# Optimization experiments

Hardware: AMD Instinct MI355X
Metric: run time of the kernel (lower is better)

Reference implementation:

```python
import jax, jax.numpy as jnp
import numpy as np

EPS = 1e-6
GROUPS = 32  # min(C//4, 32) with C=256

def group_norm(x, scale, bias):
    B, H, W, C = x.shape
    g = GROUPS
    xg = x.reshape(B, H, W, g, C // g)
    mean = jnp.mean(xg, axis=(1, 2, 4), keepdims=True)
    var = jnp.var(xg, axis=(1, 2, 4), keepdims=True)
    xg = (xg - mean) * jax.lax.rsqrt(var + EPS)
    return xg.reshape(B, H, W, C) * scale + bias

def nin(x, w, b):
    return jnp.einsum('bhwc,cd->bhwd', x, w) + b

def setup_inputs() -> dict:
    key = jax.random.key(0)
    ks = jax.random.split(key, 11)
    B, H, W, C = 8, 64, 64, 256
    s = 1.0 / np.sqrt(C)
    return {
        'x': jax.random.normal(ks[0], (B, H, W, C), jnp.float32),
        'gn_scale': jnp.ones((C,), jnp.float32),
        'gn_bias': jnp.zeros((C,), jnp.float32),
        'Wq': jax.random.normal(ks[1], (C, C), jnp.float32) * s,
        'bq': jnp.zeros((C,), jnp.float32),
        'Wk': jax.random.normal(ks[2], (C, C), jnp.float32) * s,
        'bk': jnp.zeros((C,), jnp.float32),
        'Wv': jax.random.normal(ks[3], (C, C), jnp.float32) * s,
        'bv': jnp.zeros((C,), jnp.float32),
        'Wo': jax.random.normal(ks[4], (C, C), jnp.float32) * s * 0.1,
        'bo': jnp.zeros((C,), jnp.float32),
    }

def reference(x, gn_scale, gn_bias, Wq, bq, Wk, bk, Wv, bv, Wo, bo):
    B, H, W, C = x.shape
    h = group_norm(x, gn_scale, gn_bias)
    q = nin(h, Wq, bq)
    k = nin(h, Wk, bk)
    v = nin(h, Wv, bv)
    w = jnp.einsum('bhwc,bHWc->bhwHW', q, k) * (C ** -0.5)
    w = w.reshape(B, H, W, H * W)
    w = jax.nn.softmax(w, axis=-1)
    w = w.reshape(B, H, W, H, W)
    h = jnp.einsum('bhwHW,bHWc->bhwc', w, v)
    h = nin(h, Wo, bo)
    return x + h
```

## Files before the change

kernel.cpp:

```cpp
#include <hip/hip_runtime.h>
#include <stdint.h>

using short8 = __attribute__((ext_vector_type(8))) short;
using f32x4  = __attribute__((ext_vector_type(4))) float;

#define L2E 1.44269504088896f

static __device__ __forceinline__ unsigned short f2bf(float f) {
  union { float f; uint32_t u; } v; v.f = f;
  uint32_t r = v.u + 0x7fffu + ((v.u >> 16) & 1u);
  return (unsigned short)(r >> 16);
}
static __device__ __forceinline__ float bf2f(unsigned short u) {
  union { uint32_t u; float f; } v; v.u = ((uint32_t)u) << 16;
  return v.f;
}

static __device__ __forceinline__ void gload16(const unsigned short* g, unsigned short* l) {
  __builtin_amdgcn_global_load_lds(
      (const __attribute__((address_space(1))) void*)g,
      (__attribute__((address_space(3))) void*)l, 16, 0, 0);
}

static __device__ __forceinline__ float red_add_lg(float x) {
  x += __shfl_xor(x, 16);
  x += __shfl_xor(x, 32);
  return x;
}
static __device__ __forceinline__ float red_max_lg(float x) {
  x = fmaxf(x, __shfl_xor(x, 16));
  x = fmaxf(x, __shfl_xor(x, 32));
  return x;
}

__global__ __launch_bounds__(256) void prep_w(
    const float* __restrict__ Wq, const float* __restrict__ Wk,
    const float* __restrict__ Wv, const float* __restrict__ Wo,
    unsigned short* __restrict__ Wt) {
  int k = threadIdx.x, d = blockIdx.x, w = blockIdx.y;
  const float* src = (w==0)?Wq:(w==1)?Wk:(w==2)?Wv:Wo;
  Wt[w*65536 + d*256 + k] = f2bf(src[k*256 + d]);
}

__global__ __launch_bounds__(256) void gn_stats(
    const float* __restrict__ x, float* __restrict__ part) {
  int c = threadIdx.x, ch = blockIdx.x, b = blockIdx.y;
  float s = 0.f, q = 0.f;
  const float* p = x + ((b*4096) + ch*64)*256 + c;
  for (int it = 0; it < 64; ++it) {
    float v = p[it*256];
    s += v; q += v*v;
  }
  s += __shfl_xor(s,1); q += __shfl_xor(q,1);
  s += __shfl_xor(s,2); q += __shfl_xor(q,2);
  s += __shfl_xor(s,4); q += __shfl_xor(q,4);
  if ((c & 7) == 0) {
    int g = c >> 3;
    part[((b*64 + ch)*32 + g)*2 + 0] = s;
    part[((b*64 + ch)*32 + g)*2 + 1] = q;
  }
}

__global__ __launch_bounds__(256) void gn_apply(
    const float* __restrict__ x, const float* __restrict__ part,
    const float* __restrict__ sc, const float* __restrict__ bi,
    unsigned short* __restrict__ h) {
  int c = threadIdx.x, ch = blockIdx.x, b = blockIdx.y;
  int g = c >> 3;
  float s = 0.f, q = 0.f;
  for (int cc = 0; cc < 64; ++cc) {
    s += part[((b*64 + cc)*32 + g)*2 + 0];
    q += part[((b*64 + cc)*32 + g)*2 + 1];
  }
  float mean = s * (1.f/32768.f);
  float var  = q * (1.f/32768.f) - mean*mean;
  float rstd = rsqrtf(var + 1e-6f);
  float a  = rstd * sc[c];
  float d0 = bi[c] - mean * a;
  const float* p = x + ((b*4096) + ch*64)*256 + c;
  unsigned short* o = h + ((b*4096) + ch*64)*256 + c;
  for (int it = 0; it < 64; ++it)
    o[it*256] = f2bf(p[it*256] * a + d0);
}

__global__ __launch_bounds__(256) void gemm_qk(
    const unsigned short* __restrict__ A,
    const unsigned short* __restrict__ Wtq,
    const unsigned short* __restrict__ Wtk,
    const float* __restrict__ bq,
    const float* __restrict__ bk,
    unsigned short* __restrict__ Qout,
    unsigned short* __restrict__ Kout) {
  int tid = threadIdx.x;
  int w = tid >> 6, l = tid & 63, lr = l & 15, lg = l >> 4;
  int i0 = blockIdx.x * 64;
  int j0 = w * 64;
  f32x4 accq[4][4] = {}, acck[4][4] = {};
#pragma unroll
  for (int kk = 0; kk < 8; ++kk) {
    short8 af[4], bfq[4], bfk[4];
#pragma unroll
    for (int mi = 0; mi < 4; ++mi)
      af[mi] = *(const short8*)(A + (i0 + mi*16 + lr)*256 + kk*32 + lg*8);
#pragma unroll
    for (int ni = 0; ni < 4; ++ni) {
      bfq[ni] = *(const short8*)(Wtq + (j0 + ni*16 + lr)*256 + kk*32 + lg*8);
      bfk[ni] = *(const short8*)(Wtk + (j0 + ni*16 + lr)*256 + kk*32 + lg*8);
    }
#pragma unroll
    for (int mi = 0; mi < 4; ++mi)
#pragma unroll
      for (int ni = 0; ni < 4; ++ni) {
        accq[mi][ni] = __builtin_amdgcn_mfma_f32_16x16x32_bf16(af[mi], bfq[ni], accq[mi][ni], 0,0,0);
        acck[mi][ni] = __builtin_amdgcn_mfma_f32_16x16x32_bf16(af[mi], bfk[ni], acck[mi][ni], 0,0,0);
      }
  }
#pragma unroll
  for (int mi = 0; mi < 4; ++mi) {
#pragma unroll
    for (int ni = 0; ni < 4; ++ni) {
      int j = j0 + ni*16 + lr;
#pragma unroll
      for (int r = 0; r < 4; ++r) {
        int i = i0 + mi*16 + lg*4 + r;
        Qout[i*256 + j] = f2bf((accq[mi][ni][r] + bq[j]) * 0.0625f);
        Kout[i*256 + j] = f2bf(acck[mi][ni][r] + bk[j]);
      }
    }
  }
}

__global__ __launch_bounds__(256) void gemm_bt(
    const unsigned short* __restrict__ A,
    const unsigned short* __restrict__ Bm,
    const float* __restrict__ bias_n,
    const float* __restrict__ bias_m,
    const float* __restrict__ resid,
    void* __restrict__ outp, float scale, int mode) {
  int tid = threadIdx.x;
  int w = tid >> 6, l = tid & 63, lr = l & 15, lg = l >> 4;
  int i0 = blockIdx.x * 64;
  int j0 = blockIdx.y * 256 + w * 64;
  f32x4 acc[4][4] = {};
#pragma unroll
  for (int kk = 0; kk < 8; ++kk) {
    short8 af[4], bfr[4];
#pragma unroll
    for (int mi = 0; mi < 4; ++mi)
      af[mi] = *(const short8*)(A + (i0 + mi*16 + lr)*256 + kk*32 + lg*8);
#pragma unroll
    for (int ni = 0; ni < 4; ++ni)
      bfr[ni] = *(const short8*)(Bm + (j0 + ni*16 + lr)*256 + kk*32 + lg*8);
#pragma unroll
    for (int mi = 0; mi < 4; ++mi)
#pragma unroll
      for (int ni = 0; ni < 4; ++ni)
        acc[mi][ni] = __builtin_amdgcn_mfma_f32_16x16x32_bf16(af[mi], bfr[ni], acc[mi][ni], 0,0,0);
  }
#pragma unroll
  for (int mi = 0; mi < 4; ++mi) {
#pragma unroll
    for (int ni = 0; ni < 4; ++ni) {
      int j = j0 + ni*16 + lr;
#pragma unroll
      for (int r = 0; r < 4; ++r) {
        int i = i0 + mi*16 + lg*4 + r;
        float v = acc[mi][ni][r];
        if (mode == 0) {
          ((unsigned short*)outp)[i*256 + j] = f2bf((v + bias_n[j]) * scale);
        } else if (mode == 1) {
          int idx = ((j >> 12) << 20) + i*4096 + (j & 4095);
          ((unsigned short*)outp)[idx] = f2bf(v + bias_m[i]);
        } else {
          ((float*)outp)[i*256 + j] = v + bias_n[j] + resid[i*256 + j];
        }
      }
    }
  }
}

static __device__ __forceinline__ void stage_kv32(
    const unsigned short* __restrict__ Kb, const unsigned short* __restrict__ Vb,
    int kt, unsigned short* dK, unsigned short* dV, int w, int l) {
#pragma unroll
  for (int i = 0; i < 4; ++i) {
    int t = (w*4 + i)*64 + l;
    int r = t >> 5, cs = t & 31;
    int cg = cs ^ (r & 7);
    gload16(Kb + (kt*32 + r)*256 + cg*8, dK + t*8);
  }
#pragma unroll
  for (int i = 0; i < 4; ++i) {
    int t = (w*4 + i)*64 + l;
    int d = t >> 2, s = t & 3;
    int sg = s ^ ((d ^ (d >> 2)) & 3);
    gload16(Vb + d*4096 + kt*32 + sg*8, dV + t*8);
  }
}

__global__ __launch_bounds__(256, 2) void attn_fwd(
    const unsigned short* __restrict__ Q,
    const unsigned short* __restrict__ Kmat,
    const unsigned short* __restrict__ Vt,
    unsigned short* __restrict__ P0,
    unsigned short* __restrict__ P1,
    float* __restrict__ stats) {
  __shared__ __align__(16) unsigned short ldsK[2][32][256];
  __shared__ __align__(16) unsigned short ldsV[2][256][32];

  int tid = threadIdx.x;
  int w = tid >> 6, l = tid & 63, lr = l & 15, lg = l >> 4;
  int b  = blockIdx.x & 7;
  int mt = (blockIdx.x >> 3) & 31;
  int ks = blockIdx.x >> 8;
  int m0 = mt*128 + w*32;
  int sw = lr & 7;
  int vsw = (lr ^ (lr >> 2)) & 3;
  int lgp = ((lg & 1) << 1) | (lg >> 1);

  const unsigned short* Kb = Kmat + b*(4096*256) + ks*(2048*256);
  const unsigned short* Vb = Vt   + (b << 20) + ks*2048;
  unsigned short* Pp = ks ? P1 : P0;

  short8 qf[2][8];
#pragma unroll
  for (int qn = 0; qn < 2; ++qn) {
    int qbase = ((b*4096) + m0 + qn*16 + lr)*256 + lg*8;
#pragma unroll
    for (int kk = 0; kk < 8; ++kk)
      qf[qn][kk] = *(const short8*)(Q + qbase + kk*32);
  }

  float mrun[2], lrun[2];
  f32x4 oacc[2][16] = {};
  mrun[0] = mrun[1] = -1e30f;
  lrun[0] = lrun[1] = 0.f;

  stage_kv32(Kb, Vb, 0, &ldsK[0][0][0], &ldsV[0][0][0], w, l);

  for (int kt = 0; kt < 64; ++kt) {
    int cur = kt & 1;
    if (kt < 63) {
      stage_kv32(Kb, Vb, kt+1, &ldsK[cur^1][0][0], &ldsV[cur^1][0][0], w, l);
      asm volatile("s_waitcnt vmcnt(8)" ::: "memory");
    } else {
      asm volatile("s_waitcnt vmcnt(0)" ::: "memory");
    }
    __builtin_amdgcn_s_barrier();
    __builtin_amdgcn_sched_barrier(0);

    const unsigned short (*Kc)[256] = ldsK[cur];
    const unsigned short (*Vc)[32]  = ldsV[cur];

    f32x4 s_[2][2];
#pragma unroll
    for (int qn = 0; qn < 2; ++qn)
#pragma unroll
      for (int kn = 0; kn < 2; ++kn) s_[qn][kn] = (f32x4){0.f,0.f,0.f,0.f};
#pragma unroll
    for (int kn = 0; kn < 2; ++kn) {
#pragma unroll
      for (int kk = 0; kk < 8; ++kk) {
        short8 kf = *(const short8*)&Kc[kn*16 + lr][((kk*4 + lg) ^ sw)*8];
        s_[0][kn] = __builtin_amdgcn_mfma_f32_16x16x32_bf16(kf, qf[0][kk], s_[0][kn], 0,0,0);
        s_[1][kn] = __builtin_amdgcn_mfma_f32_16x16x32_bf16(kf, qf[1][kk], s_[1][kn], 0,0,0);
      }
    }

    short8 pa[2];
#pragma unroll
    for (int qn = 0; qn < 2; ++qn) {
      float ma = fmaxf(fmaxf(s_[qn][0][0], s_[qn][0][1]), fmaxf(s_[qn][0][2], s_[qn][0][3]));
      float mb = fmaxf(fmaxf(s_[qn][1][0], s_[qn][1][1]), fmaxf(s_[qn][1][2], s_[qn][1][3]));
      float pmax = fmaxf(ma, mb);
      if (__any(pmax > mrun[qn] + 8.f)) {
        float mx = red_max_lg(pmax);
        float mnew = fmaxf(mrun[qn], mx);
        float alpha = __builtin_amdgcn_exp2f((mrun[qn] - mnew) * L2E);
        mrun[qn] = mnew;
        lrun[qn] *= alpha;
        float at[4];
#pragma unroll
        for (int r = 0; r < 4; ++r) at[r] = __shfl(alpha, lg*4 + r);
#pragma unroll
        for (int jt = 0; jt < 16; ++jt)
#pragma unroll
          for (int r = 0; r < 4; ++r) oacc[qn][jt][r] *= at[r];
      }
      float mL = mrun[qn] * L2E;
      float p[2][4];
#pragma unroll
      for (int kn = 0; kn < 2; ++kn)
#pragma unroll
        for (int r = 0; r < 4; ++r)
          p[kn][r] = __builtin_amdgcn_exp2f(s_[qn][kn][r]*L2E - mL);
      float t0 = (p[0][0]+p[0][1]) + (p[0][2]+p[0][3]);
      float t1 = (p[1][0]+p[1][1]) + (p[1][2]+p[1][3]);
      lrun[qn] += red_add_lg(t0 + t1);
      unsigned int X0, X1, Y0, Y1;
      asm("v_cvt_pk_bf16_f32 %0, %1, %2" : "=v"(X0) : "v"(p[0][0]), "v"(p[0][1]));
      asm("v_cvt_pk_bf16_f32 %0, %1, %2" : "=v"(X1) : "v"(p[0][2]), "v"(p[0][3]));
      asm("v_cvt_pk_bf16_f32 %0, %1, %2" : "=v"(Y0) : "v"(p[1][0]), "v"(p[1][1]));
      asm("v_cvt_pk_bf16_f32 %0, %1, %2" : "=v"(Y1) : "v"(p[1][2]), "v"(p[1][3]));
      asm("v_permlane16_swap_b32 %0, %1" : "+v"(X0), "+v"(Y0));
      asm("v_permlane16_swap_b32 %0, %1" : "+v"(X1), "+v"(Y1));
      union { unsigned int u[4]; short8 s8; } pk;
      pk.u[0] = X0;
      pk.u[1] = X1;
      pk.u[2] = Y0;
      pk.u[3] = Y1;
      pa[qn] = pk.s8;
    }

#pragma unroll
    for (int jt = 0; jt < 16; ++jt) {
      short8 vf = *(const short8*)&Vc[jt*16 + lr][(lgp ^ vsw)*8];
      oacc[0][jt] = __builtin_amdgcn_mfma_f32_16x16x32_bf16(pa[0], vf, oacc[0][jt], 0,0,0);
      oacc[1][jt] = __builtin_amdgcn_mfma_f32_16x16x32_bf16(pa[1], vf, oacc[1][jt], 0,0,0);
    }
    __builtin_amdgcn_sched_barrier(0);
    __builtin_amdgcn_s_barrier();
  }

  if (lg == 0) {
#pragma unroll
    for (int qn = 0; qn < 2; ++qn) {
      int row = b*4096 + m0 + qn*16 + lr;
      stats[(ks*32768 + row)*2 + 0] = mrun[qn];
      stats[(ks*32768 + row)*2 + 1] = lrun[qn];
    }
  }
#pragma unroll
  for (int qn = 0; qn < 2; ++qn) {
#pragma unroll
    for (int r = 0; r < 4; ++r) {
      int row = ((b*4096) + m0 + qn*16 + lg*4 + r)*256;
#pragma unroll
      for (int jt = 0; jt < 16; ++jt)
        Pp[row + jt*16 + lr] = f2bf(oacc[qn][jt][r]);
    }
  }
}

__global__ __launch_bounds__(256) void merge_attn(
    const unsigned short* __restrict__ P0,
    const unsigned short* __restrict__ P1,
    const float* __restrict__ stats,
    unsigned short* __restrict__ Out) {
  int tid = threadIdx.x;
  int row = blockIdx.x*8 + (tid >> 5);
  int c8  = (tid & 31) * 8;
  float m1 = stats[row*2 + 0],          l1 = stats[row*2 + 1];
  float m2 = stats[(32768 + row)*2 + 0], l2 = stats[(32768 + row)*2 + 1];
  float M  = fmaxf(m1, m2);
  float a1 = __builtin_amdgcn_exp2f((m1 - M) * L2E);
  float a2 = __builtin_amdgcn_exp2f((m2 - M) * L2E);
  float inv = 1.f / (a1*l1 + a2*l2);
  a1 *= inv; a2 *= inv;
  short8 v1 = *(const short8*)(P0 + row*256 + c8);
  short8 v2 = *(const short8*)(P1 + row*256 + c8);
  union { unsigned short u[8]; short8 s8; } o;
#pragma unroll
  for (int j = 0; j < 8; ++j)
    o.u[j] = f2bf(bf2f((unsigned short)v1[j])*a1 + bf2f((unsigned short)v2[j])*a2);
  *(short8*)(Out + row*256 + c8) = o.s8;
}

extern "C" void kernel_launch(void* const* d_in, const int* in_sizes, int n_in,
                              void* d_out, int out_size, void* d_ws, size_t ws_size,
                              hipStream_t stream) {
  (void)in_sizes; (void)n_in; (void)out_size; (void)ws_size;
  const float* x  = (const float*)d_in[0];
  const float* gs = (const float*)d_in[1];
  const float* gb = (const float*)d_in[2];
  const float* Wq = (const float*)d_in[3];
  const float* bq = (const float*)d_in[4];
  const float* Wk = (const float*)d_in[5];
  const float* bk = (const float*)d_in[6];
  const float* Wv = (const float*)d_in[7];
  const float* bv = (const float*)d_in[8];
  const float* Wo = (const float*)d_in[9];
  const float* bo = (const float*)d_in[10];

  char* ws = (char*)d_ws;
  unsigned short* h  = (unsigned short*)(ws);
  unsigned short* Qb = (unsigned short*)(ws + (size_t)16777216);
  unsigned short* Kb = (unsigned short*)(ws + (size_t)33554432);
  unsigned short* Vt = (unsigned short*)(ws + (size_t)50331648);
  unsigned short* Wt = (unsigned short*)(ws + (size_t)67108864);
  float* part        = (float*)(ws + (size_t)67108864 + 524288);
  float* stats       = (float*)(ws + (size_t)67108864 + 524288 + 131072);
  unsigned short* Op1 = (unsigned short*)d_out;

  prep_w  <<<dim3(256,4), 256, 0, stream>>>(Wq, Wk, Wv, Wo, Wt);
  gn_stats<<<dim3(64,8),  256, 0, stream>>>(x, part);
  gn_apply<<<dim3(64,8),  256, 0, stream>>>(x, part, gs, gb, h);
  gemm_qk<<<dim3(512,1), 256, 0, stream>>>(h, Wt, Wt+65536, bq, bk, Qb, Kb);
  gemm_bt<<<dim3(4,128), 256, 0, stream>>>(Wt+131072, h, nullptr, bv, nullptr, Vt, 1.0f, 1);
  attn_fwd<<<dim3(512),  256, 0, stream>>>(Qb, Kb, Vt, h, Op1, stats);
  merge_attn<<<dim3(4096), 256, 0, stream>>>(h, Op1, stats, Qb);
  gemm_bt<<<dim3(512,1), 256, 0, stream>>>(Qb, Wt+196608, bo, nullptr, x, d_out, 1.0f, 2);
}
```

Baseline: 325.6 us.

## Fuse group-norm apply into QK and V projection GEMM operand loads

Replaces the gn_apply kernel, which wrote a normalized bf16 copy of the activations, with a tiny per-batch coefficient kernel. The QK and V projection GEMMs now read fp32 x directly and apply the scale/shift and bf16 conversion while building MFMA fragments. This removes one full write and re-read of the normalized tensor, at the cost of reading fp32 (twice the bytes) in both GEMMs. The attention kernel also precomputes its K/V staging offsets once instead of recomputing them each tile.

```diff
diff --git a/kernel.cpp b/kernel.cpp
--- a/kernel.cpp
+++ b/kernel.cpp
@@ -31,6 +31,28 @@
   x = fmaxf(x, __shfl_xor(x, 16));
   x = fmaxf(x, __shfl_xor(x, 32));
   return x;
+}
+
+static __device__ __forceinline__ short8 gn_frag(
+    const float* __restrict__ xp, f32x4 ca0, f32x4 ca1, f32x4 cd0, f32x4 cd1) {
+  f32x4 x0 = *(const f32x4*)xp;
+  f32x4 x1 = *(const f32x4*)(xp + 4);
+  float g0 = fmaf(x0[0], ca0[0], cd0[0]);
+  float g1 = fmaf(x0[1], ca0[1], cd0[1]);
+  float g2 = fmaf(x0[2], ca0[2], cd0[2]);
+  float g3 = fmaf(x0[3], ca0[3], cd0[3]);
+  float g4 = fmaf(x1[0], ca1[0], cd1[0]);
+  float g5 = fmaf(x1[1], ca1[1], cd1[1]);
+  float g6 = fmaf(x1[2], ca1[2], cd1[2]);
+  float g7 = fmaf(x1[3], ca1[3], cd1[3]);
+  unsigned int u0, u1, u2, u3;
+  asm("v_cvt_pk_bf16_f32 %0, %1, %2" : "=v"(u0) : "v"(g0), "v"(g1));
+  asm("v_cvt_pk_bf16_f32 %0, %1, %2" : "=v"(u1) : "v"(g2), "v"(g3));
+  asm("v_cvt_pk_bf16_f32 %0, %1, %2" : "=v"(u2) : "v"(g4), "v"(g5));
+  asm("v_cvt_pk_bf16_f32 %0, %1, %2" : "=v"(u3) : "v"(g6), "v"(g7));
+  union { unsigned int u[4]; short8 s8; } pk;
+  pk.u[0] = u0; pk.u[1] = u1; pk.u[2] = u2; pk.u[3] = u3;
+  return pk.s8;
 }
 
 __global__ __launch_bounds__(256) void prep_w(
@@ -61,11 +83,11 @@
   }
 }
 
-__global__ __launch_bounds__(256) void gn_apply(
-    const float* __restrict__ x, const float* __restrict__ part,
+__global__ __launch_bounds__(256) void gn_coef(
+    const float* __restrict__ part,
     const float* __restrict__ sc, const float* __restrict__ bi,
-    unsigned short* __restrict__ h) {
-  int c = threadIdx.x, ch = blockIdx.x, b = blockIdx.y;
+    float* __restrict__ agn, float* __restrict__ dgn) {
+  int c = threadIdx.x, b = blockIdx.x;
   int g = c >> 3;
   float s = 0.f, q = 0.f;
   for (int cc = 0; cc < 64; ++cc) {
@@ -76,44 +98,144 @@
   float var  = q * (1.f/32768.f) - mean*mean;
   float rstd = rsqrtf(var + 1e-6f);
   float a  = rstd * sc[c];
-  float d0 = bi[c] - mean * a;
-  const float* p = x + ((b*4096) + ch*64)*256 + c;
-  unsigned short* o = h + ((b*4096) + ch*64)*256 + c;
-  for (int it = 0; it < 64; ++it)
-    o[it*256] = f2bf(p[it*256] * a + d0);
+  agn[b*256 + c] = a;
+  dgn[b*256 + c] = bi[c] - mean * a;
 }
 
 __global__ __launch_bounds__(256) void gemm_qk(
-    const unsigned short* __restrict__ A,
+    const float* __restrict__ x,
+    const float* __restrict__ agn, const float* __restrict__ dgn,
     const unsigned short* __restrict__ Wtq,
     const unsigned short* __restrict__ Wtk,
     const float* __restrict__ bq,
     const float* __restrict__ bk,
     unsigned short* __restrict__ Qout,
     unsigned short* __restrict__ Kout) {
+  __shared__ float aco[256], dco[256];
+  int tid = threadIdx.x;
+  int w = tid >> 6, l = tid & 63, lr = l & 15, lg = l >> 4;
+  int i0 = blockIdx.x * 64;
+  int b  = blockIdx.x >> 6;
+  int j0 = w * 64;
+  aco[tid] = agn[b*256 + tid];
+  dco[tid] = dgn[b*256 + tid];
+  __syncthreads();
+  f32x4 accq[4][4] = {}, acck[4][4] = {};
+#pragma unroll
+  for (int kk = 0; kk < 8; ++kk) {
+    int k0 = kk*32 + lg*8;
+    f32x4 ca0 = *(const f32x4*)&aco[k0];
+    f32x4 ca1 = *(const f32x4*)&aco[k0 + 4];
+    f32x4 cd0 = *(const f32x4*)&dco[k0];
+    f32x4 cd1 = *(const f32x4*)&dco[k0 + 4];
+    short8 af[4], bfq[4], bfk[4];
+#pragma unroll
+    for (int mi = 0; mi < 4; ++mi)
+      af[mi] = gn_frag(x + (i0 + mi*16 + lr)*256 + k0, ca0, ca1, cd0, cd1);
+#pragma unroll
+    for (int ni = 0; ni < 4; ++ni) {
+      bfq[ni] = *(const short8*)(Wtq + (j0 + ni*16 + lr)*256 + k0);
+      bfk[ni] = *(const short8*)(Wtk + (j0 + ni*16 + lr)*256 + k0);
+    }
+#pragma unroll
+    for (int mi = 0; mi < 4; ++mi)
+#pragma unroll
+      for (int ni = 0; ni < 4; ++ni) {
+        accq[mi][ni] = __builtin_amdgcn_mfma_f32_16x16x32_bf16(af[mi], bfq[ni], accq[mi][ni], 0,0,0);
+        acck[mi][ni] = __builtin_amdgcn_mfma_f32_16x16x32_bf16(af[mi], bfk[ni], acck[mi][ni], 0,0,0);
+      }
+  }
+#pragma unroll
+  for (int mi = 0; mi < 4; ++mi) {
+#pragma unroll
+    for (int ni = 0; ni < 4; ++ni) {
+      int j = j0 + ni*16 + lr;
+#pragma unroll
+      for (int r = 0; r < 4; ++r) {
+        int i = i0 + mi*16 + lg*4 + r;
+        Qout[i*256 + j] = f2bf((accq[mi][ni][r] + bq[j]) * 0.0625f);
+        Kout[i*256 + j] = f2bf(acck[mi][ni][r] + bk[j]);
+      }
+    }
+  }
+}
+
+__global__ __launch_bounds__(256) void gemm_vt(
+    const unsigned short* __restrict__ Wtv,
+    const float* __restrict__ x,
+    const float* __restrict__ agn, const float* __restrict__ dgn,
+    const float* __restrict__ bv,
+    unsigned short* __restrict__ Vt) {
+  __shared__ float aco[256], dco[256];
+  int tid = threadIdx.x;
+  int w = tid >> 6, l = tid & 63, lr = l & 15, lg = l >> 4;
+  int i0 = blockIdx.x * 64;
+  int j0 = blockIdx.y * 256 + w * 64;
+  int b  = blockIdx.y >> 4;
+  aco[tid] = agn[b*256 + tid];
+  dco[tid] = dgn[b*256 + tid];
+  __syncthreads();
+  f32x4 acc[4][4] = {};
+#pragma unroll
+  for (int kk = 0; kk < 8; ++kk) {
+    int k0 = kk*32 + lg*8;
+    f32x4 ca0 = *(const f32x4*)&aco[k0];
+    f32x4 ca1 = *(const f32x4*)&aco[k0 + 4];
+    f32x4 cd0 = *(const f32x4*)&dco[k0];
+    f32x4 cd1 = *(const f32x4*)&dco[k0 + 4];
+    short8 af[4], bfr[4];
+#pragma unroll
+    for (int mi = 0; mi < 4; ++mi)
+      af[mi] = *(const short8*)(Wtv + (i0 + mi*16 + lr)*256 + k0);
+#pragma unroll
+    for (int ni = 0; ni < 4; ++ni)
+      bfr[ni] = gn_frag(x + (j0 + ni*16 + lr)*256 + k0, ca0, ca1, cd0, cd1);
+#pragma unroll
+    for (int mi = 0; mi < 4; ++mi)
+#pragma unroll
+      for (int ni = 0; ni < 4; ++ni)
+        acc[mi][ni] = __builtin_amdgcn_mfma_f32_16x16x32_bf16(af[mi], bfr[ni], acc[mi][ni], 0,0,0);
+  }
+#pragma unroll
+  for (int mi = 0; mi < 4; ++mi) {
+#pragma unroll
+    for (int ni = 0; ni < 4; ++ni) {
+      int j = j0 + ni*16 + lr;
+#pragma unroll
+      for (int r = 0; r < 4; ++r) {
+        int i = i0 + mi*16 + lg*4 + r;
+        int idx = ((j >> 12) << 20) + i*4096 + (j & 4095);
+        Vt[idx] = f2bf(acc[mi][ni][r] + bv[i]);
+      }
+    }
+  }
+}
+
+__global__ __launch_bounds__(256) void gemm_bt(
+    const unsigned short* __restrict__ A,
+    const unsigned short* __restrict__ Bm,
+    const float* __restrict__ bias_n,
+    const float* __restrict__ resid,
+    float* __restrict__ outp) {
   int tid = threadIdx.x;
   int w = tid >> 6, l = tid & 63, lr = l & 15, lg = l >> 4;
   int i0 = blockIdx.x * 64;
   int j0 = w * 64;
-  f32x4 accq[4][4] = {}, acck[4][4] = {};
+  f32x4 acc[4][4] = {};
 #pragma unroll
   for (int kk = 0; kk < 8; ++kk) {
-    short8 af[4], bfq[4], bfk[4];
+    short8 af[4], bfr[4];
 #pragma unroll
     for (int mi = 0; mi < 4; ++mi)
       af[mi] = *(const short8*)(A + (i0 + mi*16 + lr)*256 + kk*32 + lg*8);
 #pragma unroll
-    for (int ni = 0; ni < 4; ++ni) {
-      bfq[ni] = *(const short8*)(Wtq + (j0 + ni*16 + lr)*256 + kk*32 + lg*8);
-      bfk[ni] = *(const short8*)(Wtk + (j0 + ni*16 + lr)*256 + kk*32 + lg*8);
-    }
-#pragma unroll
-    for (int mi = 0; mi < 4; ++mi)
-#pragma unroll
-      for (int ni = 0; ni < 4; ++ni) {
-        accq[mi][ni] = __builtin_amdgcn_mfma_f32_16x16x32_bf16(af[mi], bfq[ni], accq[mi][ni], 0,0,0);
-        acck[mi][ni] = __builtin_amdgcn_mfma_f32_16x16x32_bf16(af[mi], bfk[ni], acck[mi][ni], 0,0,0);
-      }
+    for (int ni = 0; ni < 4; ++ni)
+      bfr[ni] = *(const short8*)(Bm + (j0 + ni*16 + lr)*256 + kk*32 + lg*8);
+#pragma unroll
+    for (int mi = 0; mi < 4; ++mi)
+#pragma unroll
+      for (int ni = 0; ni < 4; ++ni)
+        acc[mi][ni] = __builtin_amdgcn_mfma_f32_16x16x32_bf16(af[mi], bfr[ni], acc[mi][ni], 0,0,0);
   }
 #pragma unroll
   for (int mi = 0; mi < 4; ++mi) {
@@ -123,78 +245,9 @@
 #pragma unroll
       for (int r = 0; r < 4; ++r) {
         int i = i0 + mi*16 + lg*4 + r;
-        Qout[i*256 + j] = f2bf((accq[mi][ni][r] + bq[j]) * 0.0625f);
-        Kout[i*256 + j] = f2bf(acck[mi][ni][r] + bk[j]);
-      }
-    }
-  }
-}
-
-__global__ __launch_bounds__(256) void gemm_bt(
-    const unsigned short* __restrict__ A,
-    const unsigned short* __restrict__ Bm,
-    const float* __restrict__ bias_n,
-    const float* __restrict__ bias_m,
-    const float* __restrict__ resid,
-    void* __restrict__ outp, float scale, int mode) {
-  int tid = threadIdx.x;
-  int w = tid >> 6, l = tid & 63, lr = l & 15, lg = l >> 4;
-  int i0 = blockIdx.x * 64;
-  int j0 = blockIdx.y * 256 + w * 64;
-  f32x4 acc[4][4] = {};
-#pragma unroll
-  for (int kk = 0; kk < 8; ++kk) {
-    short8 af[4], bfr[4];
-#pragma unroll
-    for (int mi = 0; mi < 4; ++mi)
-      af[mi] = *(const short8*)(A + (i0 + mi*16 + lr)*256 + kk*32 + lg*8);
-#pragma unroll
-    for (int ni = 0; ni < 4; ++ni)
-      bfr[ni] = *(const short8*)(Bm + (j0 + ni*16 + lr)*256 + kk*32 + lg*8);
-#pragma unroll
-    for (int mi = 0; mi < 4; ++mi)
-#pragma unroll
-      for (int ni = 0; ni < 4; ++ni)
-        acc[mi][ni] = __builtin_amdgcn_mfma_f32_16x16x32_bf16(af[mi], bfr[ni], acc[mi][ni], 0,0,0);
-  }
-#pragma unroll
-  for (int mi = 0; mi < 4; ++mi) {
-#pragma unroll
-    for (int ni = 0; ni < 4; ++ni) {
-      int j = j0 + ni*16 + lr;
-#pragma unroll
-      for (int r = 0; r < 4; ++r) {
-        int i = i0 + mi*16 + lg*4 + r;
-        float v = acc[mi][ni][r];
-        if (mode == 0) {
-          ((unsigned short*)outp)[i*256 + j] = f2bf((v + bias_n[j]) * scale);
-        } else if (mode == 1) {
-          int idx = ((j >> 12) << 20) + i*4096 + (j & 4095);
-          ((unsigned short*)outp)[idx] = f2bf(v + bias_m[i]);
-        } else {
-          ((float*)outp)[i*256 + j] = v + bias_n[j] + resid[i*256 + j];
-        }
-      }
-    }
-  }
-}
-
-static __device__ __forceinline__ void stage_kv32(
-    const unsigned short* __restrict__ Kb, const unsigned short* __restrict__ Vb,
-    int kt, unsigned short* dK, unsigned short* dV, int w, int l) {
-#pragma unroll
-  for (int i = 0; i < 4; ++i) {
-    int t = (w*4 + i)*64 + l;
-    int r = t >> 5, cs = t & 31;
-    int cg = cs ^ (r & 7);
-    gload16(Kb + (kt*32 + r)*256 + cg*8, dK + t*8);
-  }
-#pragma unroll
-  for (int i = 0; i < 4; ++i) {
-    int t = (w*4 + i)*64 + l;
-    int d = t >> 2, s = t & 3;
-    int sg = s ^ ((d ^ (d >> 2)) & 3);
-    gload16(Vb + d*4096 + kt*32 + sg*8, dV + t*8);
+        outp[i*256 + j] = acc[mi][ni][r] + bias_n[j] + resid[i*256 + j];
+      }
+    }
   }
 }
 
@@ -222,6 +275,17 @@
   const unsigned short* Vb = Vt   + (b << 20) + ks*2048;
   unsigned short* Pp = ks ? P1 : P0;
 
+  int koff[4], voff[4], dst[4];
+#pragma unroll
+  for (int i = 0; i < 4; ++i) {
+    int t = (w*4 + i)*64 + l;
+    int r = t >> 5, cs = t & 31;
+    koff[i] = r*256 + (cs ^ (r & 7))*8;
+    int d = t >> 2, s = t & 3;
+    voff[i] = d*4096 + (s ^ ((d ^ (d >> 2)) & 3))*8;
+    dst[i]  = t*8;
+  }
+
   short8 qf[2][8];
 #pragma unroll
   for (int qn = 0; qn < 2; ++qn) {
@@ -236,12 +300,22 @@
   mrun[0] = mrun[1] = -1e30f;
   lrun[0] = lrun[1] = 0.f;
 
-  stage_kv32(Kb, Vb, 0, &ldsK[0][0][0], &ldsV[0][0][0], w, l);
+#pragma unroll
+  for (int i = 0; i < 4; ++i) gload16(Kb + koff[i], &ldsK[0][0][0] + dst[i]);
+#pragma unroll
+  for (int i = 0; i < 4; ++i) gload16(Vb + voff[i], &ldsV[0][0][0] + dst[i]);
 
   for (int kt = 0; kt < 64; ++kt) {
     int cur = kt & 1;
     if (kt < 63) {
-      stage_kv32(Kb, Vb, kt+1, &ldsK[cur^1][0][0], &ldsV[cur^1][0][0], w, l);
+      const unsigned short* Kn = Kb + (kt + 1)*8192;
+      const unsigned short* Vn = Vb + (kt + 1)*32;
+      unsigned short* dK = &ldsK[cur^1][0][0];
+      unsigned short* dV = &ldsV[cur^1][0][0];
+#pragma unroll
+      for (int i = 0; i < 4; ++i) gload16(Kn + koff[i], dK + dst[i]);
+#pragma unroll
+      for (int i = 0; i < 4; ++i) gload16(Vn + voff[i], dV + dst[i]);
       asm volatile("s_waitcnt vmcnt(8)" ::: "memory");
     } else {
       asm volatile("s_waitcnt vmcnt(0)" ::: "memory");
@@ -305,10 +379,7 @@
       asm("v_permlane16_swap_b32 %0, %1" : "+v"(X0), "+v"(Y0));
       asm("v_permlane16_swap_b32 %0, %1" : "+v"(X1), "+v"(Y1));
       union { unsigned int u[4]; short8 s8; } pk;
-      pk.u[0] = X0;
-      pk.u[1] = X1;
-      pk.u[2] = Y0;
-      pk.u[3] = Y1;
+      pk.u[0] = X0; pk.u[1] = X1; pk.u[2] = Y0; pk.u[3] = Y1;
       pa[qn] = pk.s8;
     }
 
@@ -390,14 +461,16 @@
   unsigned short* Wt = (unsigned short*)(ws + (size_t)67108864);
   float* part        = (float*)(ws + (size_t)67108864 + 524288);
   float* stats       = (float*)(ws + (size_t)67108864 + 524288 + 131072);
+  float* agn = (float*)ws;
+  float* dgn = (float*)(ws + 8192);
   unsigned short* Op1 = (unsigned short*)d_out;
 
   prep_w  <<<dim3(256,4), 256, 0, stream>>>(Wq, Wk, Wv, Wo, Wt);
   gn_stats<<<dim3(64,8),  256, 0, stream>>>(x, part);
-  gn_apply<<<dim3(64,8),  256, 0, stream>>>(x, part, gs, gb, h);
-  gemm_qk<<<dim3(512,1), 256, 0, stream>>>(h, Wt, Wt+65536, bq, bk, Qb, Kb);
-  gemm_bt<<<dim3(4,128), 256, 0, stream>>>(Wt+131072, h, nullptr, bv, nullptr, Vt, 1.0f, 1);
+  gn_coef <<<dim3(8),     256, 0, stream>>>(part, gs, gb, agn, dgn);
+  gemm_qk<<<dim3(512,1), 256, 0, stream>>>(x, agn, dgn, Wt, Wt+65536, bq, bk, Qb, Kb);
+  gemm_vt<<<dim3(4,128), 256, 0, stream>>>(Wt+131072, x, agn, dgn, bv, Vt);
   attn_fwd<<<dim3(512),  256, 0, stream>>>(Qb, Kb, Vt, h, Op1, stats);
   merge_attn<<<dim3(4096), 256, 0, stream>>>(h, Op1, stats, Qb);
-  gemm_bt<<<dim3(512,1), 256, 0, stream>>>(Qb, Wt+196608, bo, nullptr, x, d_out, 1.0f, 2);
-}
+  gemm_bt<<<dim3(512,1), 256, 0, stream>>>(Qb, Wt+196608, bo, x, (float*)d_out);
+}
```

Result: slower. 338.4 us (+3.9%).
